# Performance work log

Hardware: AMD Instinct MI355X
Metric: run time of the kernel (lower is better)

Reference implementation:

```python
import jax, jax.numpy as jnp
import numpy as np
from jax import lax

C = 64      # channel
IMG = 21    # img_size (h = w)
D = 441     # d = IMG*IMG, odd
P = 25      # padsize = sqrt(spe_head)*sqrt(share_head) = 5*5
PS = 4      # pad_space = P - IMG
PAD1 = 220  # d // 2
START = 2   # pad_space // 2


def _unfold5(x):
    # torch nn.Unfold(kernel_size=(5,5), dilation=5) on (b, c, 25, 25) -> (b, c*25, 25)
    # input row = ph + 5*i with ph,i in [0,5): reshape rows/cols into (i, ph), (j, pw)
    b, c = x.shape[0], x.shape[1]
    xr = x.reshape(b, c, 5, 5, 5, 5)                      # (b, c, i, ph, j, pw)
    return xr.transpose(0, 1, 2, 4, 3, 5).reshape(b, c * 25, 25)


def setup_inputs() -> dict:
    key = jax.random.key(0)
    ks = jax.random.split(key, 9)
    def n(k, shape, s=0.05):
        return jax.random.normal(k, shape, dtype=jnp.float32) * s
    return {
        "x": jax.random.normal(ks[0], (2, C, IMG, IMG), dtype=jnp.float32),
        "wk": n(ks[1], (D, 1, D)),          # depthwise Conv1d weight (groups=D)
        "bk": n(ks[2], (D,)),
        "w1": n(ks[3], (25, 25, 50)),       # grouped 1x1 conv: (group, out_per_grp, in_per_grp)
        "bn_gamma": jnp.ones((25, 25), jnp.float32),
        "bn_beta": jnp.zeros((25, 25), jnp.float32),
        "bn_mean": jnp.zeros((25, 25), jnp.float32),
        "bn_var": jnp.ones((25, 25), jnp.float32),
        "w2": n(ks[4], (25, D, 25)),        # grouped 1x1 conv: (group, out_per_grp=D/..., in_per_grp)
        "b2": n(ks[5], (25, D)),
        "wv": n(ks[6], (C, 1, 3, 3)),       # depthwise 3x3 Conv2d weight
        "bv": n(ks[7], (C,)),
    }


def reference(x, wk, bk, w1, bn_gamma, bn_beta, bn_mean, bn_var, w2, b2, wv, bv):
    bs = x.shape[0]
    # key generation: depthwise conv1d over the channel axis, spatial positions as conv channels
    k = x.reshape(bs, C, IMG * IMG).transpose(0, 2, 1)    # (bs, 441, 64)
    k1 = lax.conv_general_dilated(k, wk, (1,), [(PAD1, PAD1)],
                                  dimension_numbers=("NCH", "OIH", "NCH"),
                                  feature_group_count=D) + bk[None, :, None]
    k1 = k1.transpose(0, 2, 1).reshape(bs, C, IMG, IMG)
    k1_pad = jnp.pad(k1, ((0, 0), (0, 0), (0, PS), (0, PS)))   # (bs, C, 25, 25)
    q_pad = jnp.pad(x, ((0, 0), (0, 0), (0, PS), (0, PS)))
    key_cols = _unfold5(k1_pad).transpose(0, 2, 1)             # (bs, 25, C*25)
    q_cols = _unfold5(q_pad).transpose(0, 2, 1)
    key_q = jnp.stack((q_cols, key_cols), axis=2).reshape(bs, 50, 25, C)
    kq = key_q.reshape(bs, 25, 50, C)                          # (bs, groups, in_per_grp, c)
    # attention_embed: grouped 1x1 conv -> BN(eval) -> ReLU -> grouped 1x1 conv
    att = jnp.einsum("goi,bgic->bgoc", w1, kq)                 # (bs, 25, 25, C)
    inv = bn_gamma * lax.rsqrt(bn_var + 1e-5)
    att = jax.nn.relu((att - bn_mean[None, :, :, None]) * inv[None, :, :, None]
                      + bn_beta[None, :, :, None])
    att = jnp.einsum("goi,bgic->bgoc", w2, att) + b2[None, :, :, None]   # (bs, 25, 441, C)
    att = jnp.tile(att, (1, 25, 1, 1)).transpose(0, 3, 1, 2)             # (bs, C, 625, 441)
    att = att.reshape(bs, C, 5, 5, 5, 5, D)
    att = jnp.swapaxes(att, 3, 4).reshape(bs, C, P, P, D)
    att = jax.nn.softmax(att, axis=-1).transpose(0, 1, 4, 2, 3)          # (bs, C, 441, 25, 25)
    # value path: depthwise 3x3 conv, asymmetric pad, sliding windows over channel axis
    v = lax.conv_general_dilated(x, wv, (1, 1), [(1, 1), (1, 1)],
                                 dimension_numbers=("NCHW", "OIHW", "NCHW"),
                                 feature_group_count=C) + bv[None, :, None, None]
    pad_v = jnp.pad(v, ((0, 0), (PAD1, PAD1), (PS, 0), (PS, 0)))  # (bs, 504, 25, 25)
    vf = pad_v.reshape(bs, C + D - 1, P * P)
    idx = jnp.arange(C)[:, None] + jnp.arange(D)[None, :]          # (64, 441) window indices
    vw = vf[:, idx, :].reshape(bs, C, D, P, P)
    temp = jnp.einsum("bcdhw,bcdhw->bchw", vw, att)                # multiply + sum over d
    out = temp + k1_pad
    return out[:, :, START:START + IMG, START:START + IMG]
```

## Files before the change

### kernel.cpp

```cpp
#include <hip/hip_runtime.h>

#define BVO 28224

__global__ __launch_bounds__(512) void semca_kernel(
    const float* __restrict__ x,  const float* __restrict__ wk, const float* __restrict__ bk,
    const float* __restrict__ w1,
    const float* __restrict__ bn_gamma, const float* __restrict__ bn_beta,
    const float* __restrict__ bn_mean,  const float* __restrict__ bn_var,
    const float* __restrict__ w2, const float* __restrict__ b2,
    const float* __restrict__ wvw, const float* __restrict__ bv,
    float* __restrict__ out)
{
    int blk = blockIdx.x;
    int b = blk / 25, g = blk % 25;
    int ph = g / 5, pw = g % 5;
    int tid  = threadIdx.x;
    int lane = tid & 63;
    int wvid = tid >> 6;

    __shared__ float L[14592];
    float* k1s  = L;
    float* att1 = L + 1600;
    float* smM  = L + 3200;
    float* smR  = L + 3264;
    float* redm = L + 3328;
    float* redz = L + 3840;
    float* sv   = L + 3328;
    float* xs   = L + 4352;
    float* kq   = L + 5952;
    float* w1s  = L + 9152;
    float* ws2  = L + 5952;
    float* b2s  = L + 9152;
    float* wTt  = L + 10402;

    for (int idx = tid; idx < 1600; idx += 512) {
        int p = idx >> 6, c = idx & 63;
        int row = 5*(p/5) + ph, col = 5*(p%5) + pw;
        float v0 = 0.f;
        if (row < 21 && col < 21) v0 = x[b*BVO + c*441 + row*21 + col];
        xs[idx] = v0;
    }
    for (int idx = tid; idx < 1250; idx += 512) w1s[idx] = w1[g*1250 + idx];
    __syncthreads();

    for (int p = wvid; p < 25; p += 8) {
        int row = 5*(p/5) + ph, col = 5*(p%5) + pw;
        float acc = 0.f;
        if (row < 21 && col < 21) {
            int d = row*21 + col;
            const float* wkp = wk + d*441 + 220 - lane;
            acc = bk[d];
            #pragma unroll
            for (int cp = 0; cp < 64; ++cp)
                acc += xs[p*64 + cp] * wkp[cp];
        }
        k1s[p*64 + lane] = acc;
    }
    __syncthreads();

    for (int idx = tid; idx < 3200; idx += 512) {
        int m = idx >> 6, e = idx & 63;
        int B = (m < 25) ? m : m - 25;
        int u = (B << 6) + e;
        int c = u / 25, p = u - 25*c;
        kq[idx] = (m < 25) ? xs[p*64 + c] : k1s[p*64 + c];
    }
    __syncthreads();

    {
        float kqcol[50];
        #pragma unroll
        for (int m = 0; m < 50; ++m) kqcol[m] = kq[m*64 + lane];
        #pragma unroll
        for (int k = 0; k < 4; ++k) {
            int o = wvid + 8*k;
            if (o < 25) {
                float acc = 0.f;
                #pragma unroll
                for (int m = 0; m < 50; ++m) acc += w1s[o*50 + m] * kqcol[m];
                float inv = bn_gamma[g*25+o] * rsqrtf(bn_var[g*25+o] + 1e-5f);
                acc = (acc - bn_mean[g*25+o]) * inv + bn_beta[g*25+o];
                att1[o*64 + lane] = fmaxf(acc, 0.f);
            }
        }
    }
    __syncthreads();

    for (int idx = tid; idx < 3175; idx += 512) ws2[idx] = w2[g*11025 + 157*25 + idx];
    if (tid < 127) b2s[tid] = b2[g*441 + 157 + tid];

    float a1r[25];
    #pragma unroll
    for (int i = 0; i < 25; ++i) a1r[i] = att1[i*64 + lane];

    const float* w2g = w2 + g*11025;
    const float* b2g = b2 + g*441;
    float mxA = -1e30f, zA = 0.f, mxB = -1e30f, zB = 0.f;
    for (int k = 0; k < 54; k += 2) {
        int o2a = __builtin_amdgcn_readfirstlane(wvid + 8*k);
        int o2b = o2a + 8;
        const float* wpa = w2g + o2a*25;
        const float* wpb = w2g + o2b*25;
        float va = b2g[o2a], vb = b2g[o2b];
        #pragma unroll
        for (int i = 0; i < 25; ++i) { va += wpa[i]*a1r[i]; vb += wpb[i]*a1r[i]; }
        float na = fmaxf(mxA, va);
        zA = zA * __expf(mxA - na) + __expf(va - na); mxA = na;
        float nb = fmaxf(mxB, vb);
        zB = zB * __expf(mxB - nb) + __expf(vb - nb); mxB = nb;
    }
    {
        int o2a = __builtin_amdgcn_readfirstlane(wvid + 432);
        const float* wpa = w2g + o2a*25;
        float va = b2g[o2a];
        #pragma unroll
        for (int i = 0; i < 25; ++i) va += wpa[i]*a1r[i];
        float na = fmaxf(mxA, va);
        zA = zA * __expf(mxA - na) + __expf(va - na); mxA = na;
    }
    if (wvid == 0) {
        const float* wpb = w2g + 440*25;
        float vb = b2g[440];
        #pragma unroll
        for (int i = 0; i < 25; ++i) vb += wpb[i]*a1r[i];
        float nb = fmaxf(mxB, vb);
        zB = zB * __expf(mxB - nb) + __expf(vb - nb); mxB = nb;
    }
    float mx = fmaxf(mxA, mxB);
    float zz = zA * __expf(mxA - mx) + zB * __expf(mxB - mx);

    redm[wvid*64 + lane] = mx;
    redz[wvid*64 + lane] = zz;
    __syncthreads();
    if (wvid == 0) {
        float M = -1e30f;
        #pragma unroll
        for (int w = 0; w < 8; ++w) M = fmaxf(M, redm[w*64 + lane]);
        float Z = 0.f;
        #pragma unroll
        for (int w = 0; w < 8; ++w) Z += redz[w*64 + lane] * __expf(redm[w*64 + lane] - M);
        smM[lane] = M;
        smR[lane] = 1.f / Z;
    }
    __syncthreads();

    {
        float Me = smM[lane], Re = smR[lane];
        int s = (lane & 15) << 2;
        #pragma unroll
        for (int k = 0; k < 8; ++k) {
            int cv = wvid + 8*k;
            int r = cv + 63 - lane;
            const float* wp = ws2 + r*25;
            float acc = b2s[r];
            #pragma unroll
            for (int i = 0; i < 25; ++i) acc += wp[i] * a1r[i];
            wTt[lane*64 + (cv ^ s)] = __expf(acc - Me) * Re;
        }
    }
    __syncthreads();

    int y0 = (ph + 3) % 5, x0 = (pw + 3) % 5;
    int ny = (21 - y0 + 4) / 5, nx = (21 - x0 + 4) / 5;
    int npix = ny * nx;
    for (int k = 0; k < 4; ++k) {
        int p = wvid + 8*k;
        if (p >= npix) continue;
        int yy = y0 + 5*(p / nx), xx = x0 + 5*(p % nx);
        float vt = 0.f;
        if (yy >= 2 && xx >= 2) {
            int vy = yy - 2, vx = xx - 2;
            float vval = bv[lane];
            const float* xp = x + b*BVO + lane*441;
            #pragma unroll
            for (int ky = 0; ky < 3; ++ky) {
                int r2 = vy + ky - 1;
                if (r2 < 0 || r2 >= 21) continue;
                #pragma unroll
                for (int kx = 0; kx < 3; ++kx) {
                    int c2 = vx + kx - 1;
                    if (c2 < 0 || c2 >= 21) continue;
                    vval += xp[r2*21 + c2] * wvw[lane*9 + ky*3 + kx];
                }
            }
            sv[wvid*64 + lane] = vval;
            const float4* wrow = (const float4*)(wTt + lane*64);
            int s4 = lane & 15;
            #pragma unroll
            for (int q4 = 0; q4 < 16; ++q4) {
                float4 w4 = wrow[q4 ^ s4];
                int cv0 = q4 * 4;
                vt += sv[wvid*64 + cv0 + 0] * w4.x;
                vt += sv[wvid*64 + cv0 + 1] * w4.y;
                vt += sv[wvid*64 + cv0 + 2] * w4.z;
                vt += sv[wvid*64 + cv0 + 3] * w4.w;
            }
        }
        int pk = ((yy + 2 - ph) / 5) * 5 + ((xx + 2 - pw) / 5);
        float kt = k1s[pk*64 + lane];
        out[b*BVO + lane*441 + yy*21 + xx] = kt + vt;
    }
}

extern "C" void kernel_launch(void* const* d_in, const int* in_sizes, int n_in,
                              void* d_out, int out_size, void* d_ws, size_t ws_size,
                              hipStream_t stream) {
    const float* x        = (const float*)d_in[0];
    const float* wk       = (const float*)d_in[1];
    const float* bk       = (const float*)d_in[2];
    const float* w1       = (const float*)d_in[3];
    const float* bn_gamma = (const float*)d_in[4];
    const float* bn_beta  = (const float*)d_in[5];
    const float* bn_mean  = (const float*)d_in[6];
    const float* bn_var   = (const float*)d_in[7];
    const float* w2       = (const float*)d_in[8];
    const float* b2       = (const float*)d_in[9];
    const float* wv       = (const float*)d_in[10];
    const float* bv       = (const float*)d_in[11];

    float* out = (float*)d_out;

    hipLaunchKernelGGL(semca_kernel, dim3(50), dim3(512), 0, stream,
                       x, wk, bk, w1, bn_gamma, bn_beta, bn_mean, bn_var,
                       w2, b2, wv, bv, out);
}
```

Before: 40.72 us.

## Split fused kernel into three stages to parallelize w2 projection and softmax

Measured after the change: 38.69 us. 1.05x faster.

```diff
diff --git a/kernel.cpp b/kernel.cpp
--- a/kernel.cpp
+++ b/kernel.cpp
@@ -2,170 +2,170 @@
 
 #define BVO 28224
 
-__global__ __launch_bounds__(512) void semca_kernel(
-    const float* __restrict__ x,  const float* __restrict__ wk, const float* __restrict__ bk,
+
+__global__ __launch_bounds__(256) void kA(
+    const float* __restrict__ x, const float* __restrict__ wk, const float* __restrict__ bk,
     const float* __restrict__ w1,
     const float* __restrict__ bn_gamma, const float* __restrict__ bn_beta,
     const float* __restrict__ bn_mean,  const float* __restrict__ bn_var,
-    const float* __restrict__ w2, const float* __restrict__ b2,
-    const float* __restrict__ wvw, const float* __restrict__ bv,
+    float* __restrict__ k1g, float* __restrict__ att1g)
+{
+    int blk = blockIdx.x;
+    int b = blk / 25, g = blk % 25;
+    int ph = g / 5, pw = g % 5;
+    int tid = threadIdx.x, lane = tid & 63, wv = tid >> 6;
+
+    __shared__ float xs[1600];
+    __shared__ float k1u[1600];
+
+    for (int u = tid; u < 1600; u += 256) {
+        int c = u / 25, p = u - 25 * c;
+        int row = 5*(p/5) + ph, col = 5*(p%5) + pw;
+        xs[u] = (row < 21 && col < 21) ? x[b*BVO + c*441 + row*21 + col] : 0.f;
+    }
+    __syncthreads();
+
+    for (int k = 0; k < 7; ++k) {
+        int p = wv + 4*k;
+        if (p >= 25) break;
+        int row = 5*(p/5) + ph, col = 5*(p%5) + pw;
+        float acc = 0.f;
+        if (row < 21 && col < 21) {
+            int d = row*21 + col;
+            const float* wkp = wk + d*441 + 220 - lane;
+            float a0 = 0.f, a1 = 0.f;
+            #pragma unroll
+            for (int cp = 0; cp < 64; cp += 2) {
+                a0 += xs[25*cp + p]       * wkp[cp];
+                a1 += xs[25*(cp+1) + p]   * wkp[cp+1];
+            }
+            acc = bk[d] + a0 + a1;
+        }
+        k1u[lane*25 + p] = acc;
+        k1g[blk*1600 + p*64 + lane] = acc;
+    }
+    __syncthreads();
+
+    float kq[50];
+    #pragma unroll
+    for (int m = 0; m < 25; ++m) kq[m] = xs[m*64 + lane];
+    #pragma unroll
+    for (int m = 0; m < 25; ++m) kq[25+m] = k1u[m*64 + lane];
+
+    const float* w1g = w1 + g*1250;
+    for (int k = 0; k < 7; ++k) {
+        int o = wv + 4*k;
+        if (o >= 25) break;
+        const float* wp = w1g + o*50;
+        float a0 = 0.f, a1 = 0.f;
+        #pragma unroll
+        for (int m = 0; m < 50; m += 2) { a0 += wp[m]*kq[m]; a1 += wp[m+1]*kq[m+1]; }
+        float acc = a0 + a1;
+        float inv = bn_gamma[g*25+o] * rsqrtf(bn_var[g*25+o] + 1e-5f);
+        acc = (acc - bn_mean[g*25+o]) * inv + bn_beta[g*25+o];
+        att1g[blk*1600 + o*64 + lane] = fmaxf(acc, 0.f);
+    }
+}
+
+__global__ __launch_bounds__(256) void kB(
+    const float* __restrict__ att1g, const float* __restrict__ w2,
+    const float* __restrict__ b2,
+    float* __restrict__ att2c, float* __restrict__ pm, float* __restrict__ pz)
+{
+    int blk = blockIdx.x;
+    int ch = blk & 7, bg = blk >> 3;
+    int g  = bg % 25;
+    int tid = threadIdx.x, lane = tid & 63, wv = tid >> 6;
+
+    float a1r[25];
+    #pragma unroll
+    for (int i = 0; i < 25; ++i) a1r[i] = att1g[bg*1600 + i*64 + lane];
+
+    int base = __builtin_amdgcn_readfirstlane(56*ch + 14*wv);
+    const float* w2g = w2 + g*11025 + base*25;
+    const float* b2g = b2 + g*441 + base;
+
+    float vals[14];
+    #pragma unroll
+    for (int j = 0; j < 14; ++j) {
+        int r = base + j;
+        if (r < 441) {
+            const float* wp = w2g + j*25;
+            float a0 = 0.f, a1 = 0.f;
+            #pragma unroll
+            for (int i = 0; i < 24; i += 2) { a0 += wp[i]*a1r[i]; a1 += wp[i+1]*a1r[i+1]; }
+            vals[j] = b2g[j] + a0 + a1 + wp[24]*a1r[24];
+            if (r >= 157 && r < 284)
+                att2c[(bg*127 + (r-157))*64 + lane] = vals[j];
+        } else {
+            vals[j] = -1e30f;
+        }
+    }
+
+    float mx = vals[0];
+    #pragma unroll
+    for (int j = 1; j < 14; ++j) mx = fmaxf(mx, vals[j]);
+
+    __shared__ float red[4][64];
+    red[wv][lane] = mx;
+    __syncthreads();
+    float M = fmaxf(fmaxf(red[0][lane], red[1][lane]), fmaxf(red[2][lane], red[3][lane]));
+    float z = 0.f;
+    #pragma unroll
+    for (int j = 0; j < 14; ++j) z += __expf(vals[j] - M);
+    __syncthreads();
+    red[wv][lane] = z;
+    __syncthreads();
+    if (wv == 0) {
+        float Z = red[0][lane] + red[1][lane] + red[2][lane] + red[3][lane];
+        pm[blk*64 + lane] = M;
+        pz[blk*64 + lane] = Z;
+    }
+}
+
+__global__ __launch_bounds__(256) void kC(
+    const float* __restrict__ x, const float* __restrict__ wvw, const float* __restrict__ bv,
+    const float* __restrict__ k1g, const float* __restrict__ att2c,
+    const float* __restrict__ pm, const float* __restrict__ pz,
     float* __restrict__ out)
 {
     int blk = blockIdx.x;
     int b = blk / 25, g = blk % 25;
     int ph = g / 5, pw = g % 5;
-    int tid  = threadIdx.x;
-    int lane = tid & 63;
-    int wvid = tid >> 6;
-
-    __shared__ float L[14592];
-    float* k1s  = L;
-    float* att1 = L + 1600;
-    float* smM  = L + 3200;
-    float* smR  = L + 3264;
-    float* redm = L + 3328;
-    float* redz = L + 3840;
-    float* sv   = L + 3328;
-    float* xs   = L + 4352;
-    float* kq   = L + 5952;
-    float* w1s  = L + 9152;
-    float* ws2  = L + 5952;
-    float* b2s  = L + 9152;
-    float* wTt  = L + 10402;
-
-    for (int idx = tid; idx < 1600; idx += 512) {
-        int p = idx >> 6, c = idx & 63;
-        int row = 5*(p/5) + ph, col = 5*(p%5) + pw;
-        float v0 = 0.f;
-        if (row < 21 && col < 21) v0 = x[b*BVO + c*441 + row*21 + col];
-        xs[idx] = v0;
-    }
-    for (int idx = tid; idx < 1250; idx += 512) w1s[idx] = w1[g*1250 + idx];
-    __syncthreads();
-
-    for (int p = wvid; p < 25; p += 8) {
-        int row = 5*(p/5) + ph, col = 5*(p%5) + pw;
-        float acc = 0.f;
-        if (row < 21 && col < 21) {
-            int d = row*21 + col;
-            const float* wkp = wk + d*441 + 220 - lane;
-            acc = bk[d];
-            #pragma unroll
-            for (int cp = 0; cp < 64; ++cp)
-                acc += xs[p*64 + cp] * wkp[cp];
-        }
-        k1s[p*64 + lane] = acc;
-    }
-    __syncthreads();
-
-    for (int idx = tid; idx < 3200; idx += 512) {
-        int m = idx >> 6, e = idx & 63;
-        int B = (m < 25) ? m : m - 25;
-        int u = (B << 6) + e;
-        int c = u / 25, p = u - 25*c;
-        kq[idx] = (m < 25) ? xs[p*64 + c] : k1s[p*64 + c];
-    }
-    __syncthreads();
-
-    {
-        float kqcol[50];
-        #pragma unroll
-        for (int m = 0; m < 50; ++m) kqcol[m] = kq[m*64 + lane];
-        #pragma unroll
-        for (int k = 0; k < 4; ++k) {
-            int o = wvid + 8*k;
-            if (o < 25) {
-                float acc = 0.f;
-                #pragma unroll
-                for (int m = 0; m < 50; ++m) acc += w1s[o*50 + m] * kqcol[m];
-                float inv = bn_gamma[g*25+o] * rsqrtf(bn_var[g*25+o] + 1e-5f);
-                acc = (acc - bn_mean[g*25+o]) * inv + bn_beta[g*25+o];
-                att1[o*64 + lane] = fmaxf(acc, 0.f);
-            }
-        }
-    }
-    __syncthreads();
-
-    for (int idx = tid; idx < 3175; idx += 512) ws2[idx] = w2[g*11025 + 157*25 + idx];
-    if (tid < 127) b2s[tid] = b2[g*441 + 157 + tid];
-
-    float a1r[25];
-    #pragma unroll
-    for (int i = 0; i < 25; ++i) a1r[i] = att1[i*64 + lane];
-
-    const float* w2g = w2 + g*11025;
-    const float* b2g = b2 + g*441;
-    float mxA = -1e30f, zA = 0.f, mxB = -1e30f, zB = 0.f;
-    for (int k = 0; k < 54; k += 2) {
-        int o2a = __builtin_amdgcn_readfirstlane(wvid + 8*k);
-        int o2b = o2a + 8;
-        const float* wpa = w2g + o2a*25;
-        const float* wpb = w2g + o2b*25;
-        float va = b2g[o2a], vb = b2g[o2b];
-        #pragma unroll
-        for (int i = 0; i < 25; ++i) { va += wpa[i]*a1r[i]; vb += wpb[i]*a1r[i]; }
-        float na = fmaxf(mxA, va);
-        zA = zA * __expf(mxA - na) + __expf(va - na); mxA = na;
-        float nb = fmaxf(mxB, vb);
-        zB = zB * __expf(mxB - nb) + __expf(vb - nb); mxB = nb;
-    }
-    {
-        int o2a = __builtin_amdgcn_readfirstlane(wvid + 432);
-        const float* wpa = w2g + o2a*25;
-        float va = b2g[o2a];
-        #pragma unroll
-        for (int i = 0; i < 25; ++i) va += wpa[i]*a1r[i];
-        float na = fmaxf(mxA, va);
-        zA = zA * __expf(mxA - na) + __expf(va - na); mxA = na;
-    }
-    if (wvid == 0) {
-        const float* wpb = w2g + 440*25;
-        float vb = b2g[440];
-        #pragma unroll
-        for (int i = 0; i < 25; ++i) vb += wpb[i]*a1r[i];
-        float nb = fmaxf(mxB, vb);
-        zB = zB * __expf(mxB - nb) + __expf(vb - nb); mxB = nb;
-    }
-    float mx = fmaxf(mxA, mxB);
-    float zz = zA * __expf(mxA - mx) + zB * __expf(mxB - mx);
-
-    redm[wvid*64 + lane] = mx;
-    redz[wvid*64 + lane] = zz;
-    __syncthreads();
-    if (wvid == 0) {
+    int tid = threadIdx.x, lane = tid & 63, wv = tid >> 6;
+
+    __shared__ float a2s[8128];
+    __shared__ float wT[4096];
+    __shared__ float smM[64], smR[64];
+
+    for (int i = tid; i < 8128; i += 256) a2s[i] = att2c[blk*8128 + i];
+    if (tid < 64) {
         float M = -1e30f;
         #pragma unroll
-        for (int w = 0; w < 8; ++w) M = fmaxf(M, redm[w*64 + lane]);
+        for (int c = 0; c < 8; ++c) M = fmaxf(M, pm[(blk*8 + c)*64 + tid]);
         float Z = 0.f;
         #pragma unroll
-        for (int w = 0; w < 8; ++w) Z += redz[w*64 + lane] * __expf(redm[w*64 + lane] - M);
-        smM[lane] = M;
-        smR[lane] = 1.f / Z;
-    }
-    __syncthreads();
-
-    {
-        float Me = smM[lane], Re = smR[lane];
-        int s = (lane & 15) << 2;
-        #pragma unroll
-        for (int k = 0; k < 8; ++k) {
-            int cv = wvid + 8*k;
-            int r = cv + 63 - lane;
-            const float* wp = ws2 + r*25;
-            float acc = b2s[r];
-            #pragma unroll
-            for (int i = 0; i < 25; ++i) acc += wp[i] * a1r[i];
-            wTt[lane*64 + (cv ^ s)] = __expf(acc - Me) * Re;
-        }
+        for (int c = 0; c < 8; ++c)
+            Z += pz[(blk*8 + c)*64 + tid] * __expf(pm[(blk*8 + c)*64 + tid] - M);
+        smM[tid] = M;
+        smR[tid] = 1.f / Z;
+    }
+    __syncthreads();
+
+    float Me = smM[lane], Re = smR[lane];
+    #pragma unroll
+    for (int k = 0; k < 16; ++k) {
+        int cv = wv + 4*k;
+        wT[cv*64 + lane] = __expf(a2s[(cv + 63 - lane)*64 + lane] - Me) * Re;
     }
     __syncthreads();
 
     int y0 = (ph + 3) % 5, x0 = (pw + 3) % 5;
     int ny = (21 - y0 + 4) / 5, nx = (21 - x0 + 4) / 5;
     int npix = ny * nx;
-    for (int k = 0; k < 4; ++k) {
-        int p = wvid + 8*k;
-        if (p >= npix) continue;
+    for (int k = 0; k < 7; ++k) {
+        int p = wv + 4*k;
+        if (p >= npix) break;
         int yy = y0 + 5*(p / nx), xx = x0 + 5*(p % nx);
         float vt = 0.f;
         if (yy >= 2 && xx >= 2) {
@@ -183,21 +183,14 @@
                     vval += xp[r2*21 + c2] * wvw[lane*9 + ky*3 + kx];
                 }
             }
-            sv[wvid*64 + lane] = vval;
-            const float4* wrow = (const float4*)(wTt + lane*64);
-            int s4 = lane & 15;
-            #pragma unroll
-            for (int q4 = 0; q4 < 16; ++q4) {
-                float4 w4 = wrow[q4 ^ s4];
-                int cv0 = q4 * 4;
-                vt += sv[wvid*64 + cv0 + 0] * w4.x;
-                vt += sv[wvid*64 + cv0 + 1] * w4.y;
-                vt += sv[wvid*64 + cv0 + 2] * w4.z;
-                vt += sv[wvid*64 + cv0 + 3] * w4.w;
+            #pragma unroll
+            for (int cv = 0; cv < 64; ++cv) {
+                float s = __uint_as_float(__builtin_amdgcn_readlane(__float_as_uint(vval), cv));
+                vt += s * wT[cv*64 + lane];
             }
         }
         int pk = ((yy + 2 - ph) / 5) * 5 + ((xx + 2 - pw) / 5);
-        float kt = k1s[pk*64 + lane];
+        float kt = k1g[blk*1600 + pk*64 + lane];
         out[b*BVO + lane*441 + yy*21 + xx] = kt + vt;
     }
 }
@@ -218,9 +211,17 @@
     const float* wv       = (const float*)d_in[10];
     const float* bv       = (const float*)d_in[11];
 
-    float* out = (float*)d_out;
-
-    hipLaunchKernelGGL(semca_kernel, dim3(50), dim3(512), 0, stream,
-                       x, wk, bk, w1, bn_gamma, bn_beta, bn_mean, bn_var,
-                       w2, b2, wv, bv, out);
-}
+    float* out   = (float*)d_out;
+    float* k1g   = (float*)d_ws;
+    float* att1g = k1g + 80000;
+    float* att2c = att1g + 80000;
+    float* pm    = att2c + 406400;
+    float* pz    = pm + 25600;
+
+    hipLaunchKernelGGL(kA, dim3(50), dim3(256), 0, stream,
+                       x, wk, bk, w1, bn_gamma, bn_beta, bn_mean, bn_var, k1g, att1g);
+    hipLaunchKernelGGL(kB, dim3(400), dim3(256), 0, stream,
+                       att1g, w2, b2, att2c, pm, pz);
+    hipLaunchKernelGGL(kC, dim3(50), dim3(256), 0, stream,
+                       x, wv, bv, k1g, att2c, pm, pz, out);
+}
```
